# Performance work log

Hardware: AMD Instinct MI355X
Metric: run time of the kernel (lower is better)

The kernel has to match this reference:

```python
import jax, jax.numpy as jnp
import numpy as np

B, D, H, C, HALT_H, MAX_STEPS = 8192, 2048, 1024, 1000, 32, 10
EPS = 1e-08


def setup_inputs() -> dict:
    key = jax.random.key(0)
    ks = jax.random.split(key, 12)
    s = 0.02
    return {
        "x": jax.random.normal(ks[0], (B, D), jnp.float32),
        "enc_W": jax.random.normal(ks[1], (H, D), jnp.float32) * s,
        "enc_b": jnp.zeros((H,), jnp.float32),
        "ln_g": jnp.ones((H,), jnp.float32),
        "ln_b": jnp.zeros((H,), jnp.float32),
        "W_ih": jax.random.normal(ks[2], (3 * H, H), jnp.float32) * s,
        "W_hh": jax.random.normal(ks[3], (3 * H, H), jnp.float32) * s,
        "b_ih": jnp.zeros((3 * H,), jnp.float32),
        "b_hh": jnp.zeros((3 * H,), jnp.float32),
        "cls_W": jax.random.normal(ks[4], (C, H), jnp.float32) * s,
        "cls_b": jnp.zeros((C,), jnp.float32),
        "h1_W": jax.random.normal(ks[5], (HALT_H, H), jnp.float32) * s,
        "h1_b": jnp.zeros((HALT_H,), jnp.float32),
        "h2_W": jax.random.normal(ks[6], (1, HALT_H), jnp.float32) * s,
        "h2_b": jnp.zeros((1,), jnp.float32),
    }


def _forward(x, enc_W, enc_b, ln_g, ln_b, W_ih, W_hh, b_ih, b_hh,
             cls_W, cls_b, h1_W, h1_b, h2_W, h2_b):
    # encoder: Linear -> LayerNorm -> GELU (exact)
    z = x @ enc_W.T + enc_b
    mu = jnp.mean(z, axis=-1, keepdims=True)
    var = jnp.var(z, axis=-1, keepdims=True)
    z = (z - mu) * jax.lax.rsqrt(var + 1e-05) * ln_g + ln_b
    h0 = jax.nn.gelu(z, approximate=False)

    def step(h, _):
        gi = h @ W_ih.T + b_ih   # GRUCell with input = hidden
        gh = h @ W_hh.T + b_hh
        gi_r, gi_z, gi_n = jnp.split(gi, 3, axis=-1)
        gh_r, gh_z, gh_n = jnp.split(gh, 3, axis=-1)
        r = jax.nn.sigmoid(gi_r + gh_r)
        zt = jax.nn.sigmoid(gi_z + gh_z)
        n = jnp.tanh(gi_n + r * gh_n)
        h_new = (1.0 - zt) * n + zt * h
        logits = h_new @ cls_W.T + cls_b                         # [B, C]
        halt = jax.nn.sigmoid(
            jax.nn.relu(h_new @ h1_W.T + h1_b) @ h2_W.T + h2_b
        )[:, 0]                                                   # [B]
        return h_new, (logits, halt)

    _, (logits_steps, halt_steps) = jax.lax.scan(step, h0, None, length=MAX_STEPS)
    logits_stack = jnp.transpose(logits_steps, (1, 0, 2))  # [B, T, C]
    halts_stack = jnp.transpose(halt_steps, (1, 0))        # [B, T]

    log_not_halt = jnp.log(1.0 - halts_stack + EPS)
    cumsum_log = jnp.cumsum(log_not_halt, axis=1)
    cumsum_shifted = jnp.concatenate(
        [jnp.zeros((halts_stack.shape[0], 1), halts_stack.dtype), cumsum_log[:, :-1]], axis=1)
    halt_dist = halts_stack * jnp.exp(cumsum_shifted)
    remainder = 1.0 - jnp.sum(halt_dist, axis=1, keepdims=True)
    halt_dist = jnp.concatenate(
        [halt_dist[:, :-1], halt_dist[:, -1:] + jnp.maximum(remainder, 0.0)], axis=1)

    weighted_logits = jnp.sum(halt_dist[:, :, None] * logits_stack, axis=1)  # [B, C]
    step_indices = jnp.arange(1, MAX_STEPS + 1, dtype=weighted_logits.dtype)
    expected_steps = jnp.sum(halt_dist * step_indices, axis=1)
    probs = jax.nn.softmax(weighted_logits, axis=1)
    softmax_conf = jnp.max(probs, axis=1)
    comp_uncertainty = expected_steps / MAX_STEPS
    confidence = 0.7 * softmax_conf + 0.3 * (1.0 - comp_uncertainty)
    return (weighted_logits, probs, confidence, softmax_conf,
            expected_steps, halt_dist, comp_uncertainty)


def reference(x, enc_W, enc_b, ln_g, ln_b, W_ih, W_hh, b_ih, b_hh,
              cls_W, cls_b, h1_W, h1_b, h2_W, h2_b):
    return _forward(x, enc_W, enc_b, ln_g, ln_b, W_ih, W_hh, b_ih, b_hh,
                    cls_W, cls_b, h1_W, h1_b, h2_W, h2_b)
```

## Files before the change

### kernel.cpp

```cpp
#include <hip/hip_runtime.h>
#include <hip/hip_bf16.h>

#define B_ 8192
#define D_ 2048
#define H_ 1024
#define C_ 1000
#define NSTEP 10

typedef __attribute__((ext_vector_type(8))) short short8;
typedef __attribute__((ext_vector_type(4))) float f32x4;

__device__ __forceinline__ f32x4 mfma16x16(short8 a, short8 b, f32x4 c) {
  return __builtin_amdgcn_mfma_f32_16x16x32_bf16(a, b, c, 0, 0, 0);
}

__device__ __forceinline__ void async16(void* lds_uniform, const void* gsrc) {
  __builtin_amdgcn_global_load_lds(
      (const __attribute__((address_space(1))) void*)gsrc,
      (__attribute__((address_space(3))) void*)lds_uniform, 16, 0, 0);
}

__device__ __forceinline__ float sigm(float x) { return 1.0f / (1.0f + __expf(-x)); }
__device__ __forceinline__ float tanh_fast(float x) { return 1.0f - 2.0f / (__expf(2.0f * x) + 1.0f); }
__device__ __forceinline__ float b2f(short s) {
  union { unsigned u; float f; } v; v.u = ((unsigned)(unsigned short)s) << 16; return v.f;
}
__device__ __forceinline__ unsigned short f2us(float f) {
  __hip_bfloat16 h = __float2bfloat16(f); return *(unsigned short*)&h;
}

__device__ __forceinline__ int swz(int row, int slot) {
  return (row << 7) + (((slot) ^ (row & 7)) << 4);
}

__global__ void cvt_bf16_pad(const float* __restrict__ src, __hip_bfloat16* __restrict__ dst,
                             int n4, int nsrc4) {
  int i = blockIdx.x * 256 + threadIdx.x;
  if (i >= n4) return;
  float4 v = make_float4(0.f, 0.f, 0.f, 0.f);
  if (i < nsrc4) v = ((const float4*)src)[i];
  ((ushort4*)dst)[i] = make_ushort4(f2us(v.x), f2us(v.y), f2us(v.z), f2us(v.w));
}

__global__ void cvt_gates(const float* __restrict__ Wih, const float* __restrict__ Whh,
                          __hip_bfloat16* __restrict__ dst) {
  const int i = blockIdx.x * 256 + threadIdx.x;
  const int per_gate = (H_ * H_) / 4;
  const int gate = i / per_gate, rem = i - gate * per_gate;
  float4 v;
  if (gate == 0) {
    float4 a = ((const float4*)Wih)[rem], b = ((const float4*)Whh)[rem];
    v = make_float4(a.x + b.x, a.y + b.y, a.z + b.z, a.w + b.w);
  } else if (gate == 1) {
    float4 a = ((const float4*)Wih)[per_gate + rem], b = ((const float4*)Whh)[per_gate + rem];
    v = make_float4(a.x + b.x, a.y + b.y, a.z + b.z, a.w + b.w);
  } else if (gate == 2) {
    v = ((const float4*)Wih)[2 * per_gate + rem];
  } else {
    v = ((const float4*)Whh)[2 * per_gate + rem];
  }
  ((ushort4*)dst)[i] = make_ushort4(f2us(v.x), f2us(v.y), f2us(v.z), f2us(v.w));
}

template<int EPI>
__global__ __launch_bounds__(256, 2)
void gemm_bt(const __hip_bfloat16* __restrict__ A, int lda,
             const __hip_bfloat16* __restrict__ Bt, int ldb, int K,
             const float* __restrict__ bias,
             float* __restrict__ out, int out_ld, int ncol,
             const float* __restrict__ wrow) {
  __shared__ __hip_bfloat16 sA[128 * 64];
  __shared__ __hip_bfloat16 sB[128 * 64];
  const int tid = threadIdx.x;
  const int wave = tid >> 6, lane = tid & 63;
  const int m0 = blockIdx.x * 128, n0 = blockIdx.y * 128;
  const int wm = (wave >> 1) * 64, wn = (wave & 1) * 64;
  const int lr = lane & 15;
  const int g4 = lane >> 4;
  const int srow = wave * 8 + (lane >> 3);
  const int scol = ((lane & 7) ^ ((lane >> 3) & 7)) * 8;

  f32x4 acc[4][4] = {};

  const __hip_bfloat16* Asrc = A + (size_t)(m0 + srow) * lda + scol;
  const __hip_bfloat16* Bsrc = Bt + (size_t)(n0 + srow) * ldb + scol;

  for (int k0 = 0; k0 < K; k0 += 64) {
#pragma unroll
    for (int c = 0; c < 4; ++c) {
      async16((char*)sA + c * 4096 + wave * 1024, Asrc + (size_t)(c * 32) * lda + k0);
      async16((char*)sB + c * 4096 + wave * 1024, Bsrc + (size_t)(c * 32) * ldb + k0);
    }
    __syncthreads();
#pragma unroll
    for (int ks = 0; ks < 2; ++ks) {
      const int slot = ks * 4 + g4;
      short8 af[4], bfr[4];
#pragma unroll
      for (int i = 0; i < 4; ++i) {
        af[i]  = *(const short8*)((const char*)sA + swz(wm + i * 16 + lr, slot));
        bfr[i] = *(const short8*)((const char*)sB + swz(wn + i * 16 + lr, slot));
      }
#pragma unroll
      for (int i = 0; i < 4; ++i)
#pragma unroll
        for (int j = 0; j < 4; ++j)
          acc[i][j] = mfma16x16(af[i], bfr[j], acc[i][j]);
    }
    __syncthreads();
  }

  const int rbase = (lane >> 4) * 4;
  const int cbase = lane & 15;
#pragma unroll
  for (int i = 0; i < 4; ++i) {
#pragma unroll
    for (int r = 0; r < 4; ++r) {
      const int grow = m0 + wm + i * 16 + rbase + r;
      if (EPI == 1) {
        const float ws = wrow[grow];
#pragma unroll
        for (int j = 0; j < 4; ++j) {
          const int gcol = n0 + wn + j * 16 + cbase;
          if (gcol < ncol)
            out[(size_t)grow * out_ld + gcol] = acc[i][j][r] + bias[gcol] * ws;
        }
      } else {
#pragma unroll
        for (int j = 0; j < 4; ++j) {
          const int gcol = n0 + wn + j * 16 + cbase;
          out[(size_t)grow * out_ld + gcol] = acc[i][j][r] + bias[gcol];
        }
      }
    }
  }
}

__global__ __launch_bounds__(256, 2)
void gemm_gru(const __hip_bfloat16* __restrict__ A,
              const __hip_bfloat16* __restrict__ Wc4,
              const float* __restrict__ b_ih, const float* __restrict__ b_hh,
              __hip_bfloat16* __restrict__ hnewb) {
  __shared__ __hip_bfloat16 sA[128 * 64];
  __shared__ __hip_bfloat16 sB[4 * 32 * 64];
  const int tid = threadIdx.x, wave = tid >> 6, lane = tid & 63;
  const int m0 = blockIdx.x * 128, n0 = blockIdx.y * 32;
  const int wr = wave >> 1, wc = wave & 1;
  const int lr = lane & 15;
  const int g4 = lane >> 4;
  const int srow = lane >> 3;
  const int scol = ((lane & 7) ^ ((lane >> 3) & 7)) * 8;

  f32x4 acc[4][4] = {};

  const __hip_bfloat16* Asrc = A + (size_t)(m0 + wave * 8 + srow) * H_ + scol;
  const __hip_bfloat16* Bsrc = Wc4 + (size_t)(n0 + wave * 8 + srow) * H_ + scol;

  for (int k0 = 0; k0 < H_; k0 += 64) {
#pragma unroll
    for (int c = 0; c < 4; ++c)
      async16((char*)sA + c * 4096 + wave * 1024, Asrc + (size_t)(c * 32) * H_ + k0);
#pragma unroll
    for (int g = 0; g < 4; ++g)
      async16((char*)sB + g * 4096 + wave * 1024, Bsrc + ((size_t)g << 20) + k0);
    __syncthreads();
#pragma unroll
    for (int ks = 0; ks < 2; ++ks) {
      const int slot = ks * 4 + g4;
      short8 af[4];
#pragma unroll
      for (int mi = 0; mi < 4; ++mi)
        af[mi] = *(const short8*)((const char*)sA + swz(wr * 64 + mi * 16 + lr, slot));
      short8 bf[4];
#pragma unroll
      for (int g = 0; g < 4; ++g)
        bf[g] = *(const short8*)((const char*)sB + g * 4096 + swz(wc * 16 + lr, slot));
#pragma unroll
      for (int mi = 0; mi < 4; ++mi)
#pragma unroll
        for (int g = 0; g < 4; ++g)
          acc[mi][g] = mfma16x16(af[mi], bf[g], acc[mi][g]);
    }
    __syncthreads();
  }

  const int rbase = (lane >> 4) * 4;
  const int cbase = lane & 15;
  const int gcol = n0 + wc * 16 + cbase;
  const float brz = b_ih[gcol] + b_hh[gcol];
  const float bzz = b_ih[H_ + gcol] + b_hh[H_ + gcol];
  const float bin = b_ih[2 * H_ + gcol];
  const float bhn = b_hh[2 * H_ + gcol];
#pragma unroll
  for (int mi = 0; mi < 4; ++mi) {
#pragma unroll
    for (int r = 0; r < 4; ++r) {
      const int grow = m0 + wr * 64 + mi * 16 + rbase + r;
      const size_t idx = (size_t)grow * H_ + gcol;
      const float rg = sigm(acc[mi][0][r] + brz);
      const float zg = sigm(acc[mi][1][r] + bzz);
      const float ng = tanh_fast(acc[mi][2][r] + bin + rg * (acc[mi][3][r] + bhn));
      const float hv = b2f(*(const short*)(A + idx));
      hnewb[idx] = __float2bfloat16((1.0f - zg) * ng + zg * hv);
    }
  }
}

__global__ void ln_gelu(const float* __restrict__ z, const float* __restrict__ g,
                        const float* __restrict__ bta, __hip_bfloat16* __restrict__ hb) {
  const int row = blockIdx.x, t = threadIdx.x;
  __shared__ float rs[4], rs2[4];
  float4 v = ((const float4*)(z + (size_t)row * H_))[t];
  float s = v.x + v.y + v.z + v.w;
  float s2 = v.x * v.x + v.y * v.y + v.z * v.z + v.w * v.w;
#pragma unroll
  for (int off = 32; off; off >>= 1) {
    s += __shfl_down(s, off);
    s2 += __shfl_down(s2, off);
  }
  if ((t & 63) == 0) { rs[t >> 6] = s; rs2[t >> 6] = s2; }
  __syncthreads();
  const float mu = (rs[0] + rs[1] + rs[2] + rs[3]) * (1.0f / H_);
  const float var = (rs2[0] + rs2[1] + rs2[2] + rs2[3]) * (1.0f / H_) - mu * mu;
  const float rstd = rsqrtf(var + 1e-5f);
  float4 gg = ((const float4*)g)[t];
  float4 bb = ((const float4*)bta)[t];
  float o[4], res[4];
  o[0] = (v.x - mu) * rstd * gg.x + bb.x;
  o[1] = (v.y - mu) * rstd * gg.y + bb.y;
  o[2] = (v.z - mu) * rstd * gg.z + bb.z;
  o[3] = (v.w - mu) * rstd * gg.w + bb.w;
#pragma unroll
  for (int k = 0; k < 4; ++k)
    res[k] = 0.5f * o[k] * (1.0f + erff(o[k] * 0.70710678118654752f));
  ((ushort4*)(hb + (size_t)row * H_))[t] =
      make_ushort4(f2us(res[0]), f2us(res[1]), f2us(res[2]), f2us(res[3]));
}

__global__ __launch_bounds__(256, 4)
void halt_mlp2(const __hip_bfloat16* __restrict__ hb,
               const __hip_bfloat16* __restrict__ h1Wb,
               const float* __restrict__ h1b, const float* __restrict__ h2W,
               const float* __restrict__ h2b,
               float* __restrict__ cum, float* __restrict__ psum,
               float* __restrict__ esum, float* __restrict__ wsum,
               float* __restrict__ out_hd, float* __restrict__ out_es,
               float* __restrict__ out_cu, int step) {
  const int tid = threadIdx.x, wave = tid >> 6, lane = tid & 63;
  const int m0 = (blockIdx.x * 4 + wave) * 16;
  const int lr = lane & 15, lk = (lane >> 4) * 8;

  const __hip_bfloat16* Arow = hb + (size_t)(m0 + lr) * H_ + lk;
  const __hip_bfloat16* B0 = h1Wb + (size_t)lr * H_ + lk;
  const __hip_bfloat16* B1 = h1Wb + (size_t)(16 + lr) * H_ + lk;
  f32x4 acc0 = {}, acc1 = {};
#pragma unroll 4
  for (int kk = 0; kk < H_; kk += 32) {
    short8 a  = *(const short8*)(Arow + kk);
    short8 b0 = *(const short8*)(B0 + kk);
    short8 b1 = *(const short8*)(B1 + kk);
    acc0 = mfma16x16(a, b0, acc0);
    acc1 = mfma16x16(a, b1, acc1);
  }
  const float w2a = h2W[lr], w2b = h2W[16 + lr];
  const float b1a = h1b[lr], b1b = h1b[16 + lr];
  float p[4];
#pragma unroll
  for (int q = 0; q < 4; ++q)
    p[q] = fmaxf(acc0[q] + b1a, 0.f) * w2a + fmaxf(acc1[q] + b1b, 0.f) * w2b;
#pragma unroll
  for (int m = 1; m < 16; m <<= 1) {
#pragma unroll
    for (int q = 0; q < 4; ++q) p[q] += __shfl_xor(p[q], m);
  }
  if (lr == 0) {
    const float b2 = h2b[0];
#pragma unroll
    for (int q = 0; q < 4; ++q) {
      const int rl = (lane >> 4) * 4 + q;
      const int row = m0 + rl;
      const float halt = 1.f / (1.f + expf(-(p[q] + b2)));
      float c  = (step == 0) ? 0.f : cum[row];
      float ps = (step == 0) ? 0.f : psum[row];
      float es = (step == 0) ? 0.f : esum[row];
      const float pt = halt * expf(c);
      float w;
      if (step == NSTEP - 1) {
        w = pt + fmaxf(1.f - (ps + pt), 0.f);
        es += w * (float)NSTEP;
        out_es[row] = es;
        out_cu[row] = es * (1.0f / NSTEP);
        wsum[row] = ps + w;
      } else {
        w = pt;
        es += w * (float)(step + 1);
        cum[row] = c + logf(1.f - halt + 1e-8f);
        psum[row] = ps + pt;
        esum[row] = es;
      }
      out_hd[(size_t)row * NSTEP + step] = w;
    }
  }
}

__global__ void hw_final(const __hip_bfloat16* __restrict__ hstack,
                         const float* __restrict__ out_hd,
                         __hip_bfloat16* __restrict__ hwb) {
  const int t = threadIdx.x;
  const int row = blockIdx.x * 4 + (t >> 6);
  const int c0 = (t & 63) * 16;
  const float* hd = out_hd + (size_t)row * NSTEP;
  float accv[16] = {};
#pragma unroll
  for (int s = 0; s < NSTEP; ++s) {
    const float w = hd[s];
    const short8* p = (const short8*)(hstack + ((size_t)(s + 1) * B_ + row) * H_ + c0);
    short8 a0 = p[0], a1 = p[1];
#pragma unroll
    for (int q = 0; q < 8; ++q) accv[q] += w * b2f(a0[q]);
#pragma unroll
    for (int q = 0; q < 8; ++q) accv[8 + q] += w * b2f(a1[q]);
  }
  short8 r0, r1;
#pragma unroll
  for (int q = 0; q < 8; ++q) { r0[q] = (short)f2us(accv[q]); r1[q] = (short)f2us(accv[8 + q]); }
  short8* dst = (short8*)(hwb + (size_t)row * H_ + c0);
  dst[0] = r0; dst[1] = r1;
}

__global__ void finalize(const float* __restrict__ wl, const float* __restrict__ es,
                         float* __restrict__ probs, float* __restrict__ conf,
                         float* __restrict__ sconf) {
  const int row = blockIdx.x, t = threadIdx.x;
  __shared__ float red[4], red2[4];
  float4 v = make_float4(-1e30f, -1e30f, -1e30f, -1e30f);
  float m = -1e30f;
  if (t < 250) {
    v = ((const float4*)(wl + (size_t)row * C_))[t];
    m = fmaxf(fmaxf(v.x, v.y), fmaxf(v.z, v.w));
  }
#pragma unroll
  for (int off = 32; off; off >>= 1) m = fmaxf(m, __shfl_down(m, off));
  if ((t & 63) == 0) red[t >> 6] = m;
  __syncthreads();
  m = fmaxf(fmaxf(red[0], red[1]), fmaxf(red[2], red[3]));
  float4 e = make_float4(0.f, 0.f, 0.f, 0.f);
  float s = 0.f;
  if (t < 250) {
    e.x = expf(v.x - m); e.y = expf(v.y - m); e.z = expf(v.z - m); e.w = expf(v.w - m);
    s = e.x + e.y + e.z + e.w;
  }
#pragma unroll
  for (int off = 32; off; off >>= 1) s += __shfl_down(s, off);
  if ((t & 63) == 0) red2[t >> 6] = s;
  __syncthreads();
  s = red2[0] + red2[1] + red2[2] + red2[3];
  const float inv = 1.0f / s;
  if (t < 250)
    ((float4*)(probs + (size_t)row * C_))[t] = make_float4(e.x * inv, e.y * inv, e.z * inv, e.w * inv);
  if (t == 0) {
    sconf[row] = inv;
    conf[row] = 0.7f * inv + 0.3f * (1.0f - es[row] * (1.0f / NSTEP));
  }
}

extern "C" void kernel_launch(void* const* d_in, const int* in_sizes, int n_in,
                              void* d_out, int out_size, void* d_ws, size_t ws_size,
                              hipStream_t stream) {
  (void)in_sizes; (void)n_in; (void)out_size; (void)ws_size;
  const float* x     = (const float*)d_in[0];
  const float* enc_W = (const float*)d_in[1];
  const float* enc_b = (const float*)d_in[2];
  const float* ln_g  = (const float*)d_in[3];
  const float* ln_b  = (const float*)d_in[4];
  const float* W_ih  = (const float*)d_in[5];
  const float* W_hh  = (const float*)d_in[6];
  const float* b_ih  = (const float*)d_in[7];
  const float* b_hh  = (const float*)d_in[8];
  const float* cls_W = (const float*)d_in[9];
  const float* cls_b = (const float*)d_in[10];
  const float* h1_W  = (const float*)d_in[11];
  const float* h1_b  = (const float*)d_in[12];
  const float* h2_W  = (const float*)d_in[13];
  const float* h2_b  = (const float*)d_in[14];

  char* wsp = (char*)d_ws;
  auto carve = [&](size_t n) { char* p = wsp; wsp += (n + 255) & ~(size_t)255; return p; };
  __hip_bfloat16* Wc4b   = (__hip_bfloat16*)carve((size_t)4 * H_ * H_ * 2);
  __hip_bfloat16* clsWb  = (__hip_bfloat16*)carve((size_t)1024 * 1024 * 2);
  __hip_bfloat16* encWb  = (__hip_bfloat16*)carve((size_t)H_ * D_ * 2);
  __hip_bfloat16* h1Wb   = (__hip_bfloat16*)carve((size_t)32 * H_ * 2);
  __hip_bfloat16* hstack = (__hip_bfloat16*)carve((size_t)(NSTEP + 1) * B_ * H_ * 2);
  float* cum  = (float*)carve((size_t)B_ * 4);
  float* psum = (float*)carve((size_t)B_ * 4);
  float* esum = (float*)carve((size_t)B_ * 4);
  float* wsum = (float*)carve((size_t)B_ * 4);

  const size_t SLOT = (size_t)B_ * H_;
  float* z            = (float*)(hstack + SLOT);
  __hip_bfloat16* xb  = hstack + 3 * SLOT;
  __hip_bfloat16* hwb = hstack;

  float* out = (float*)d_out;
  float* out_wl    = out;
  float* out_probs = out + (size_t)B_ * C_;
  float* out_conf  = out + (size_t)2 * B_ * C_;
  float* out_sconf = out_conf + B_;
  float* out_es    = out_sconf + B_;
  float* out_hd    = out_es + B_;
  float* out_cu    = out_hd + (size_t)B_ * NSTEP;

  dim3 blk(256);
  { int n4 = B_ * D_ / 4;       cvt_bf16_pad<<<(n4 + 255) / 256, blk, 0, stream>>>(x, xb, n4, n4); }
  { int n4 = H_ * D_ / 4;       cvt_bf16_pad<<<(n4 + 255) / 256, blk, 0, stream>>>(enc_W, encWb, n4, n4); }
  { int n4 = 4 * H_ * H_ / 4;   cvt_gates<<<(n4 + 255) / 256, blk, 0, stream>>>(W_ih, W_hh, Wc4b); }
  { int n4 = 1024 * 1024 / 4;   cvt_bf16_pad<<<(n4 + 255) / 256, blk, 0, stream>>>(cls_W, clsWb, n4, C_ * H_ / 4); }
  { int n4 = 32 * H_ / 4;       cvt_bf16_pad<<<(n4 + 255) / 256, blk, 0, stream>>>(h1_W, h1Wb, n4, n4); }

  gemm_bt<0><<<dim3(B_ / 128, H_ / 128), blk, 0, stream>>>(
      xb, D_, encWb, D_, D_, enc_b, z, H_, H_, nullptr);
  ln_gelu<<<B_, blk, 0, stream>>>(z, ln_g, ln_b, hstack);

  for (int step = 0; step < NSTEP; ++step) {
    const __hip_bfloat16* hprev = hstack + (size_t)step * SLOT;
    __hip_bfloat16* hnext = hstack + (size_t)(step + 1) * SLOT;
    gemm_gru<<<dim3(B_ / 128, H_ / 32), blk, 0, stream>>>(
        hprev, Wc4b, b_ih, b_hh, hnext);
    halt_mlp2<<<B_ / 64, blk, 0, stream>>>(
        hnext, h1Wb, h1_b, h2_W, h2_b, cum, psum, esum, wsum,
        out_hd, out_es, out_cu, step);
  }

  hw_final<<<B_ / 4, blk, 0, stream>>>(hstack, out_hd, hwb);

  gemm_bt<1><<<dim3(B_ / 128, 1024 / 128), blk, 0, stream>>>(
      hwb, H_, clsWb, H_, H_, cls_b, out_wl, C_, C_, wsum);

  finalize<<<B_, blk, 0, stream>>>(out_wl, out_es, out_probs, out_conf, out_sconf);
}
```

Before: 1.048 ms.

## Enlarge GRU GEMM tile to 256 rows and split halt MLP K across waves

```diff
diff --git a/kernel.cpp b/kernel.cpp
--- a/kernel.cpp
+++ b/kernel.cpp
@@ -136,33 +136,34 @@
   }
 }
 
-__global__ __launch_bounds__(256, 2)
+__global__ __launch_bounds__(512, 4)
 void gemm_gru(const __hip_bfloat16* __restrict__ A,
               const __hip_bfloat16* __restrict__ Wc4,
               const float* __restrict__ b_ih, const float* __restrict__ b_hh,
               __hip_bfloat16* __restrict__ hnewb) {
-  __shared__ __hip_bfloat16 sA[128 * 64];
+  __shared__ __hip_bfloat16 sA[256 * 64];
   __shared__ __hip_bfloat16 sB[4 * 32 * 64];
   const int tid = threadIdx.x, wave = tid >> 6, lane = tid & 63;
-  const int m0 = blockIdx.x * 128, n0 = blockIdx.y * 32;
-  const int wr = wave >> 1, wc = wave & 1;
+  const int m0 = blockIdx.x * 256, n0 = blockIdx.y * 32;
+  const int wm = (wave >> 1) * 64;
+  const int wc = wave & 1;
   const int lr = lane & 15;
   const int g4 = lane >> 4;
-  const int srow = lane >> 3;
   const int scol = ((lane & 7) ^ ((lane >> 3) & 7)) * 8;
 
   f32x4 acc[4][4] = {};
 
-  const __hip_bfloat16* Asrc = A + (size_t)(m0 + wave * 8 + srow) * H_ + scol;
-  const __hip_bfloat16* Bsrc = Wc4 + (size_t)(n0 + wave * 8 + srow) * H_ + scol;
+  const __hip_bfloat16* Asrc = A + (size_t)(m0 + wave * 8 + (lane >> 3)) * H_ + scol;
+  const __hip_bfloat16* Bsrc = Wc4 + ((size_t)(wave >> 2) << 20)
+                             + (size_t)(n0 + (wave & 3) * 8 + (lane >> 3)) * H_ + scol;
 
   for (int k0 = 0; k0 < H_; k0 += 64) {
 #pragma unroll
     for (int c = 0; c < 4; ++c)
-      async16((char*)sA + c * 4096 + wave * 1024, Asrc + (size_t)(c * 32) * H_ + k0);
-#pragma unroll
-    for (int g = 0; g < 4; ++g)
-      async16((char*)sB + g * 4096 + wave * 1024, Bsrc + ((size_t)g << 20) + k0);
+      async16((char*)sA + c * 8192 + wave * 1024, Asrc + (size_t)(c * 64) * H_ + k0);
+#pragma unroll
+    for (int i = 0; i < 2; ++i)
+      async16((char*)sB + i * 8192 + wave * 1024, Bsrc + ((size_t)(i * 2) << 20) + k0);
     __syncthreads();
 #pragma unroll
     for (int ks = 0; ks < 2; ++ks) {
@@ -170,7 +171,7 @@
       short8 af[4];
 #pragma unroll
       for (int mi = 0; mi < 4; ++mi)
-        af[mi] = *(const short8*)((const char*)sA + swz(wr * 64 + mi * 16 + lr, slot));
+        af[mi] = *(const short8*)((const char*)sA + swz(wm + mi * 16 + lr, slot));
       short8 bf[4];
 #pragma unroll
       for (int g = 0; g < 4; ++g)
@@ -195,7 +196,7 @@
   for (int mi = 0; mi < 4; ++mi) {
 #pragma unroll
     for (int r = 0; r < 4; ++r) {
-      const int grow = m0 + wr * 64 + mi * 16 + rbase + r;
+      const int grow = m0 + wm + mi * 16 + rbase + r;
       const size_t idx = (size_t)grow * H_ + gcol;
       const float rg = sigm(acc[mi][0][r] + brz);
       const float zg = sigm(acc[mi][1][r] + bzz);
@@ -246,28 +247,41 @@
                float* __restrict__ esum, float* __restrict__ wsum,
                float* __restrict__ out_hd, float* __restrict__ out_es,
                float* __restrict__ out_cu, int step) {
+  __shared__ float part[2][2][64][8];
   const int tid = threadIdx.x, wave = tid >> 6, lane = tid & 63;
-  const int m0 = (blockIdx.x * 4 + wave) * 16;
+  const int rowgrp = wave >> 1, khalf = wave & 1;
+  const int m0 = (blockIdx.x * 2 + rowgrp) * 16;
   const int lr = lane & 15, lk = (lane >> 4) * 8;
 
-  const __hip_bfloat16* Arow = hb + (size_t)(m0 + lr) * H_ + lk;
-  const __hip_bfloat16* B0 = h1Wb + (size_t)lr * H_ + lk;
-  const __hip_bfloat16* B1 = h1Wb + (size_t)(16 + lr) * H_ + lk;
+  const __hip_bfloat16* Arow = hb + (size_t)(m0 + lr) * H_ + khalf * 512 + lk;
+  const __hip_bfloat16* B0 = h1Wb + (size_t)lr * H_ + khalf * 512 + lk;
+  const __hip_bfloat16* B1 = h1Wb + (size_t)(16 + lr) * H_ + khalf * 512 + lk;
   f32x4 acc0 = {}, acc1 = {};
 #pragma unroll 4
-  for (int kk = 0; kk < H_; kk += 32) {
+  for (int kk = 0; kk < 512; kk += 32) {
     short8 a  = *(const short8*)(Arow + kk);
     short8 b0 = *(const short8*)(B0 + kk);
     short8 b1 = *(const short8*)(B1 + kk);
     acc0 = mfma16x16(a, b0, acc0);
     acc1 = mfma16x16(a, b1, acc1);
   }
+#pragma unroll
+  for (int q = 0; q < 4; ++q) {
+    part[rowgrp][khalf][lane][q]     = acc0[q];
+    part[rowgrp][khalf][lane][4 + q] = acc1[q];
+  }
+  __syncthreads();
+  if (khalf) return;
+
   const float w2a = h2W[lr], w2b = h2W[16 + lr];
   const float b1a = h1b[lr], b1b = h1b[16 + lr];
   float p[4];
 #pragma unroll
-  for (int q = 0; q < 4; ++q)
-    p[q] = fmaxf(acc0[q] + b1a, 0.f) * w2a + fmaxf(acc1[q] + b1b, 0.f) * w2b;
+  for (int q = 0; q < 4; ++q) {
+    const float u0 = part[rowgrp][0][lane][q]     + part[rowgrp][1][lane][q]     + b1a;
+    const float u1 = part[rowgrp][0][lane][4 + q] + part[rowgrp][1][lane][4 + q] + b1b;
+    p[q] = fmaxf(u0, 0.f) * w2a + fmaxf(u1, 0.f) * w2b;
+  }
 #pragma unroll
   for (int m = 1; m < 16; m <<= 1) {
 #pragma unroll
@@ -424,9 +438,9 @@
   for (int step = 0; step < NSTEP; ++step) {
     const __hip_bfloat16* hprev = hstack + (size_t)step * SLOT;
     __hip_bfloat16* hnext = hstack + (size_t)(step + 1) * SLOT;
-    gemm_gru<<<dim3(B_ / 128, H_ / 32), blk, 0, stream>>>(
+    gemm_gru<<<dim3(B_ / 256, H_ / 32), dim3(512), 0, stream>>>(
         hprev, Wc4b, b_ih, b_hh, hnext);
-    halt_mlp2<<<B_ / 64, blk, 0, stream>>>(
+    halt_mlp2<<<B_ / 32, blk, 0, stream>>>(
         hnext, h1Wb, h1_b, h2_W, h2_b, cum, psum, esum, wsum,
         out_hd, out_es, out_cu, step);
   }
```

Measured after the change: 974.0 us. 7.1% less time.
